# Optimization experiments

Measured on AMD Instinct MI355X. Metric: run time of the kernel, lower is better.

Reference implementation:

```python
import jax, jax.numpy as jnp
import numpy as np

HEADS = 8
K = 3            # kernel_size per axis
RPB = 2 * K - 1  # rel-pos-bias extent per axis
EPS = 1e-5


def _nbr(dim, k):
    # NATTEN-style clamped window: shift window to stay fully inside [0, dim)
    q = jnp.arange(dim)
    start = jnp.clip(q - k // 2, 0, dim - k)
    nbr = start[:, None] + jnp.arange(k)[None, :]       # (dim, k) neighbor coords
    rel = nbr - q[:, None] + (k - 1)                    # (dim, k) in [0, 2k-2]
    return nbr, rel


def _instance_norm(x):
    # InstanceNorm3d, affine=False: normalize over spatial dims per (B, C)
    m = jnp.mean(x, axis=(2, 3, 4), keepdims=True)
    v = jnp.var(x, axis=(2, 3, 4), keepdims=True)
    return (x - m) * jax.lax.rsqrt(v + EPS)


def setup_inputs() -> dict:
    key = jax.random.key(0)
    ks = jax.random.split(key, 10)
    B, C, H, W, Z = 1, 128, 32, 32, 32
    Cf = 4 * C
    s = 0.02
    return {
        "x": jax.random.normal(ks[0], (B, C, H, W, Z), jnp.float32),
        "w_qkv": jax.random.normal(ks[1], (3 * C, C), jnp.float32) * s,
        "b_qkv": jnp.zeros((3 * C,), jnp.float32),
        "rpb": jax.random.normal(ks[2], (HEADS, RPB, RPB, RPB), jnp.float32) * s,
        "w_proj": jax.random.normal(ks[3], (C, C), jnp.float32) * s,
        "b_proj": jnp.zeros((C,), jnp.float32),
        "w_ffn1": jax.random.normal(ks[4], (Cf, C), jnp.float32) * s,
        "b_ffn1": jnp.zeros((Cf,), jnp.float32),
        "w_ffn2": jax.random.normal(ks[5], (C, Cf), jnp.float32) * s,
        "b_ffn2": jnp.zeros((C,), jnp.float32),
    }


def reference(x, w_qkv, b_qkv, rpb, w_proj, b_proj, w_ffn1, b_ffn1, w_ffn2, b_ffn2):
    B, C, H, W, Z = x.shape
    hd = C // HEADS
    N = H * W * Z
    KK = K ** 3

    # ---- SAM: 3D neighborhood self-attention ----
    xt = x.reshape(B, C, N).transpose(0, 2, 1)                 # (B, N, C)
    qkv = xt @ w_qkv.T + b_qkv                                  # (B, N, 3C)
    q, k_, v = jnp.split(qkv, 3, axis=-1)
    split = lambda t: t.reshape(B, N, HEADS, hd).transpose(0, 2, 1, 3)  # (B, h, N, d)
    q, k_, v = split(q), split(k_), split(v)

    nh, rh = _nbr(H, K)
    nw, rw = _nbr(W, K)
    nz, rz = _nbr(Z, K)
    # flat neighbor token index per (h, w, z, kh, kw, kz)
    nbr = ((nh[:, None, None, :, None, None] * W
            + nw[None, :, None, None, :, None]) * Z
           + nz[None, None, :, None, None, :]).reshape(N, KK)   # (N, 27)
    # flat rel-pos-bias index
    bidx = ((rh[:, None, None, :, None, None] * RPB
             + rw[None, :, None, None, :, None]) * RPB
            + rz[None, None, :, None, None, :]).reshape(N, KK)  # (N, 27)

    kg = k_[:, :, nbr]                                          # (B, h, N, 27, d)
    vg = v[:, :, nbr]                                           # (B, h, N, 27, d)
    bias = rpb.reshape(HEADS, RPB ** 3)[:, bidx]                # (h, N, 27)

    scale = jnp.asarray(hd, x.dtype) ** -0.5
    attn = jnp.einsum('bhnd,bhnkd->bhnk', q * scale, kg) + bias
    attn = jax.nn.softmax(attn, axis=-1)
    out = jnp.einsum('bhnk,bhnkd->bhnd', attn, vg)              # (B, h, N, d)
    out = out.transpose(0, 2, 1, 3).reshape(B, N, C) @ w_proj.T + b_proj
    x5 = out.transpose(0, 2, 1).reshape(B, C, H, W, Z)

    # ---- norm_in ----
    x5 = _instance_norm(x5)

    # ---- FFN (mmcv-style, GELU, residual identity) ----
    t = x5.reshape(B, C, N).transpose(0, 2, 1)                  # (B, N, C)
    t = t + (jax.nn.gelu(t @ w_ffn1.T + b_ffn1) @ w_ffn2.T + b_ffn2)
    x5 = t.transpose(0, 2, 1).reshape(B, C, H, W, Z)

    # ---- norm_out ----
    return _instance_norm(x5)
```

## Files before the change

### kernel.cpp

```cpp
#include <hip/hip_runtime.h>
#include <hip/hip_bf16.h>
#include <math.h>

#define NPOS 32768
#define CCH  128
#define C3   384
#define CF   512
#define NSH  16

typedef __attribute__((ext_vector_type(8))) short short8;
typedef __attribute__((ext_vector_type(4))) float f32x4;

__device__ inline float bf2f(unsigned short u) {
    union { unsigned int i; float f; } x; x.i = ((unsigned int)u) << 16; return x.f;
}
__device__ inline unsigned short f2bf(float f) {
    union { float f; unsigned int i; } x; x.f = f;
    unsigned int r = x.i + 0x7FFFu + ((x.i >> 16) & 1u);
    return (unsigned short)(r >> 16);
}
__device__ inline float lo_bf(unsigned int u) {
    union { unsigned int i; float f; } x; x.i = u << 16; return x.f;
}
__device__ inline float hi_bf(unsigned int u) {
    union { unsigned int i; float f; } x; x.i = u & 0xffff0000u; return x.f;
}

template<bool GELU, bool RES, bool WF32, bool WBF>
__global__ __launch_bounds__(256) void gemm_mfma(
    const unsigned short* __restrict__ A, const unsigned short* __restrict__ B,
    const float* __restrict__ bias, const unsigned short* __restrict__ res,
    float* __restrict__ outf, unsigned short* __restrict__ outb,
    int M, int Nout, int K)
{
    __shared__ alignas(16) unsigned short As[128 * 40];
    __shared__ alignas(16) unsigned short Bs[128 * 40];

    const int tid  = threadIdx.x;
    const int lane = tid & 63;
    const int wave = tid >> 6;
    const int wm = wave & 1, wn = wave >> 1;
    const int row0 = blockIdx.y * 128;
    const int col0 = blockIdx.x * 128;

    const f32x4 fzero = {0.f, 0.f, 0.f, 0.f};
    f32x4 acc[4][4];
    #pragma unroll
    for (int i = 0; i < 4; ++i)
        #pragma unroll
        for (int j = 0; j < 4; ++j) acc[i][j] = fzero;

    const int lr = lane & 15;
    const int lk = (lane >> 4) * 8;

    for (int kt = 0; kt < K; kt += 32) {
        #pragma unroll
        for (int it = 0; it < 2; ++it) {
            const int c = tid + it * 256;
            const int r = c >> 2;
            const int p = (c & 3) * 8;
            *(uint4*)&As[r * 40 + p] = *(const uint4*)&A[(size_t)(row0 + r) * K + kt + p];
            *(uint4*)&Bs[r * 40 + p] = *(const uint4*)&B[(size_t)(col0 + r) * K + kt + p];
        }
        __syncthreads();
        short8 af[4], bfr[4];
        #pragma unroll
        for (int i = 0; i < 4; ++i)
            af[i]  = *(const short8*)&As[(wm * 64 + i * 16 + lr) * 40 + lk];
        #pragma unroll
        for (int j = 0; j < 4; ++j)
            bfr[j] = *(const short8*)&Bs[(wn * 64 + j * 16 + lr) * 40 + lk];
        #pragma unroll
        for (int i = 0; i < 4; ++i)
            #pragma unroll
            for (int j = 0; j < 4; ++j)
                acc[i][j] = __builtin_amdgcn_mfma_f32_16x16x32_bf16(
                                af[i], bfr[j], acc[i][j], 0, 0, 0);
        __syncthreads();
    }

    const int gr0 = row0 + wm * 64 + (lane >> 4) * 4;
    const int gc0 = col0 + wn * 64 + lr;
    #pragma unroll
    for (int j = 0; j < 4; ++j) {
        const int gc = gc0 + j * 16;
        const float bv = bias[gc];
        #pragma unroll
        for (int i = 0; i < 4; ++i) {
            #pragma unroll
            for (int r = 0; r < 4; ++r) {
                const int gr = gr0 + i * 16 + r;
                float v = acc[i][j][r] + bv;
                if (GELU) {
                    const float g = 0.7978845608028654f * (v + 0.044715f * v * v * v);
                    const float e = __expf(2.f * g);
                    v = v * (e / (e + 1.f));
                }
                if (RES)  v += bf2f(res[(size_t)gr * Nout + gc]);
                if (WF32) outf[(size_t)gr * Nout + gc] = v;
                if (WBF)  outb[(size_t)gr * Nout + gc] = f2bf(v);
            }
        }
    }
}

__global__ __launch_bounds__(256) void attn_tiled(
    const unsigned short* __restrict__ qkv, const float* __restrict__ rpb,
    unsigned short* __restrict__ out)
{
    __shared__ unsigned int ksu[288 * 8];
    __shared__ unsigned int vsu[288 * 8];
    __shared__ unsigned int qsu[32 * 8];
    __shared__ float logits[32 * 29];
    __shared__ float rpbs[125];
    __shared__ float sinv[32];

    const int t  = threadIdx.x;
    const int line = ((blockIdx.x & 7) << 7) + (blockIdx.x >> 3);
    const int h  = blockIdx.y;
    const int w0 = line & 31, h0 = line >> 5;
    const int n0 = (h0 << 10) + (w0 << 5);
    const int sh0 = min(max(h0 - 1, 0), 29);
    const int sw0 = min(max(w0 - 1, 0), 29);
    const int rh_off = sh0 - h0 + 2;
    const int rw_off = sw0 - w0 + 2;

    if (t < 64) {
        const int pos = t >> 1, part = t & 1;
        const uint4 raw = *(const uint4*)&qkv[(size_t)(n0 + pos) * C3 + h * 16 + part * 8];
        *(uint4*)&qsu[pos * 8 + part * 4] = raw;
    } else if (t < 192) {
        const int i = t - 64;
        if (i < 125) rpbs[i] = rpb[h * 125 + i];
    }
    for (int c = t; c < 1152; c += 256) {
        const int p = c >> 2, part = c & 3;
        const int ihw = p >> 5, z = p & 31;
        const int ih = (ihw * 11) >> 5;
        const int iw = ihw - 3 * ih;
        const int n = ((sh0 + ih) << 10) + ((sw0 + iw) << 5) + z;
        const uint4 raw = *(const uint4*)&qkv[(size_t)n * C3 + CCH + (part >> 1) * CCH
                                              + h * 16 + (part & 1) * 8];
        unsigned int* d = ((part < 2) ? ksu : vsu) + p * 8 + (part & 1) * 4;
        *(uint4*)d = raw;
    }
    __syncthreads();

    {
        const int q = t >> 3, j = t & 7;
        const int sz = min(max(q - 1, 0), 29);
        const int rz_off = sz - q + 2;
        float qf[16];
        #pragma unroll
        for (int d2 = 0; d2 < 8; ++d2) {
            const unsigned int u = qsu[q * 8 + d2];
            qf[2 * d2] = lo_bf(u); qf[2 * d2 + 1] = hi_bf(u);
        }
        float lv[4];
        int nkk = 0;
        for (int kk = j; kk < 27; kk += 8) {
            const int ihw = kk / 3, dz = kk - 3 * ihw;
            const int ih = ihw / 3,  iw = ihw - 3 * ih;
            const int p = ihw * 32 + sz + dz;
            float a = 0.f;
            #pragma unroll
            for (int d2 = 0; d2 < 8; ++d2) {
                const unsigned int u = ksu[p * 8 + d2];
                a += qf[2 * d2] * lo_bf(u) + qf[2 * d2 + 1] * hi_bf(u);
            }
            const int bidx = ((ih + rh_off) * 5 + (iw + rw_off)) * 5 + (dz + rz_off);
            lv[nkk++] = a * 0.25f + rpbs[bidx];
        }
        float mx = -1e30f;
        #pragma unroll
        for (int u = 0; u < 4; ++u) if (u < nkk) mx = fmaxf(mx, lv[u]);
        mx = fmaxf(mx, __shfl_xor(mx, 1));
        mx = fmaxf(mx, __shfl_xor(mx, 2));
        mx = fmaxf(mx, __shfl_xor(mx, 4));
        float s = 0.f;
        int u = 0;
        for (int kk = j; kk < 27; kk += 8) {
            const float e = __expf(lv[u++] - mx);
            logits[q * 29 + kk] = e;
            s += e;
        }
        s += __shfl_xor(s, 1);
        s += __shfl_xor(s, 2);
        s += __shfl_xor(s, 4);
        if (j == 0) sinv[q] = 1.f / s;
    }
    __syncthreads();

    {
        const int q = t >> 3, d2 = t & 7;
        const int sz = min(max(q - 1, 0), 29);
        float ax = 0.f, ay = 0.f;
        #pragma unroll
        for (int kk = 0; kk < 27; ++kk) {
            const int p = (kk / 3) * 32 + sz + (kk % 3);
            const float w = logits[q * 29 + kk];
            const unsigned int u = vsu[p * 8 + d2];
            ax += w * lo_bf(u); ay += w * hi_bf(u);
        }
        const float inv = sinv[q];
        const unsigned int o = ((unsigned int)f2bf(ay * inv) << 16)
                             |  (unsigned int)f2bf(ax * inv);
        *(unsigned int*)&out[(size_t)(n0 + q) * CCH + h * 16 + d2 * 2] = o;
    }
}

__global__ __launch_bounds__(256) void proj_stats_kernel(
    const unsigned short* __restrict__ attnO,
    const unsigned short* __restrict__ wproj,
    const float* __restrict__ b_proj,
    unsigned short* __restrict__ x5b,
    float* __restrict__ stats)
{
    __shared__ float red[256];

    const int t    = threadIdx.x;
    const int lane = t & 63;
    const int wn   = t >> 6;
    const int lr = lane & 15;
    const int lg = lane >> 4;
    const int lk = lg * 8;
    const int n0 = blockIdx.x * 64;
    const int sh = (blockIdx.x & (NSH - 1)) * 256;

    red[t] = 0.f;

    short8 wf[2][4];
    #pragma unroll
    for (int j = 0; j < 2; ++j)
        #pragma unroll
        for (int ks = 0; ks < 4; ++ks)
            wf[j][ks] = *(const short8*)&wproj[(wn * 32 + j * 16 + lr) * CCH + ks * 32 + lk];

    const f32x4 fzero = {0.f, 0.f, 0.f, 0.f};
    f32x4 acc[4][2];
    #pragma unroll
    for (int i = 0; i < 4; ++i)
        #pragma unroll
        for (int j = 0; j < 2; ++j) acc[i][j] = fzero;

    #pragma unroll
    for (int ks = 0; ks < 4; ++ks) {
        short8 af[4];
        #pragma unroll
        for (int i = 0; i < 4; ++i)
            af[i] = *(const short8*)&attnO[(size_t)(n0 + i * 16 + lr) * CCH + ks * 32 + lk];
        #pragma unroll
        for (int i = 0; i < 4; ++i)
            #pragma unroll
            for (int j = 0; j < 2; ++j)
                acc[i][j] = __builtin_amdgcn_mfma_f32_16x16x32_bf16(
                                af[i], wf[j][ks], acc[i][j], 0, 0, 0);
    }
    __syncthreads();

    #pragma unroll
    for (int j = 0; j < 2; ++j) {
        const int gc = wn * 32 + j * 16 + lr;
        const float bv = b_proj[gc];
        float s = 0.f, q = 0.f;
        #pragma unroll
        for (int i = 0; i < 4; ++i)
            #pragma unroll
            for (int r = 0; r < 4; ++r) {
                const int gr = i * 16 + lg * 4 + r;
                const float v = acc[i][j][r] + bv;
                s += v; q += v * v;
                x5b[(size_t)(n0 + gr) * CCH + gc] = f2bf(v);
            }
        atomicAdd(&red[gc], s);
        atomicAdd(&red[128 + gc], q);
    }
    __syncthreads();
    if (t < 128) {
        atomicAdd(&stats[sh + t],       red[t]);
        atomicAdd(&stats[sh + 128 + t], red[128 + t]);
    }
}

__global__ __launch_bounds__(256) void ffn_fused_kernel(
    const unsigned short* __restrict__ x5b,
    const unsigned short* __restrict__ w1,
    const float* __restrict__ b1,
    const unsigned short* __restrict__ w2,
    const float* __restrict__ b2,
    float* __restrict__ stats,
    float* __restrict__ tT)
{
    __shared__ alignas(16) unsigned short pool[2 * 8704];
    unsigned short* As = pool;
    unsigned short* Hs = pool + 8704;
    __shared__ float red[256];
    __shared__ float ms[128];
    __shared__ float rss[128];

    const int t    = threadIdx.x;
    const int lane = t & 63;
    const int wn   = t >> 6;
    const int lr = lane & 15;
    const int lg = lane >> 4;
    const int lk = lg * 8;
    const int n0 = blockIdx.x * 64;
    const int sh = (blockIdx.x & (NSH - 1)) * 256;
    const float invN = 1.f / (float)NPOS;
    const f32x4 fzero = {0.f, 0.f, 0.f, 0.f};

    red[t] = 0.f;
    if (t < 128) {
        float s0 = 0.f, s1 = 0.f;
        #pragma unroll
        for (int s = 0; s < NSH; ++s) {
            s0 += stats[s * 256 + t];
            s1 += stats[s * 256 + 128 + t];
        }
        const float m = s0 * invN;
        const float v = s1 * invN - m * m;
        ms[t]  = m;
        rss[t] = rsqrtf(v + 1e-5f);
    }
    uint4 px[4];
    #pragma unroll
    for (int it = 0; it < 4; ++it) {
        const int idx = t + it * 256;
        const int row = idx >> 4, c0 = (idx & 15) * 8;
        px[it] = *(const uint4*)&x5b[(size_t)(n0 + row) * CCH + c0];
    }
    __syncthreads();

    #pragma unroll
    for (int it = 0; it < 4; ++it) {
        const int idx = t + it * 256;
        const int row = idx >> 4, c0 = (idx & 15) * 8;
        unsigned int u[4] = {px[it].x, px[it].y, px[it].z, px[it].w};
        #pragma unroll
        for (int p = 0; p < 4; ++p) {
            const int c = c0 + 2 * p;
            const float a = (lo_bf(u[p]) - ms[c])     * rss[c];
            const float b = (hi_bf(u[p]) - ms[c + 1]) * rss[c + 1];
            u[p] = ((unsigned int)f2bf(b) << 16) | (unsigned int)f2bf(a);
        }
        uint4 w; w.x = u[0]; w.y = u[1]; w.z = u[2]; w.w = u[3];
        *(uint4*)&As[row * 136 + c0] = w;
    }
    __syncthreads();

    f32x4 acc[4][2];
    #pragma unroll
    for (int i = 0; i < 4; ++i)
        #pragma unroll
        for (int j = 0; j < 2; ++j) acc[i][j] = fzero;

    #pragma unroll 1
    for (int cc = 0; cc < 4; ++cc) {
        short8 w1f[2][4];
        #pragma unroll
        for (int j = 0; j < 2; ++j)
            #pragma unroll
            for (int ks = 0; ks < 4; ++ks)
                w1f[j][ks] = *(const short8*)&w1[
                    (size_t)(cc * 128 + wn * 32 + j * 16 + lr) * CCH + ks * 32 + lk];

        f32x4 hacc[4][2];
        #pragma unroll
        for (int i = 0; i < 4; ++i)
            #pragma unroll
            for (int j = 0; j < 2; ++j) hacc[i][j] = fzero;
        #pragma unroll
        for (int ks = 0; ks < 4; ++ks) {
            short8 af[4];
            #pragma unroll
            for (int i = 0; i < 4; ++i)
                af[i] = *(const short8*)&As[(i * 16 + lr) * 136 + ks * 32 + lk];
            #pragma unroll
            for (int i = 0; i < 4; ++i)
                #pragma unroll
                for (int j = 0; j < 2; ++j)
                    hacc[i][j] = __builtin_amdgcn_mfma_f32_16x16x32_bf16(
                                    af[i], w1f[j][ks], hacc[i][j], 0, 0, 0);
        }

        short8 w2f[2][4];
        #pragma unroll
        for (int j = 0; j < 2; ++j)
            #pragma unroll
            for (int ks = 0; ks < 4; ++ks)
                w2f[j][ks] = *(const short8*)&w2[
                    (size_t)(wn * 32 + j * 16 + lr) * CF + cc * 128 + ks * 32 + lk];

        #pragma unroll
        for (int j = 0; j < 2; ++j) {
            const int gc = wn * 32 + j * 16 + lr;
            const float bv = b1[cc * 128 + gc];
            #pragma unroll
            for (int i = 0; i < 4; ++i)
                #pragma unroll
                for (int r = 0; r < 4; ++r) {
                    float v = hacc[i][j][r] + bv;
                    const float g = 0.7978845608028654f * (v + 0.044715f * v * v * v);
                    const float e = __expf(2.f * g);
                    v = v * (e / (e + 1.f));
                    Hs[(i * 16 + lg * 4 + r) * 136 + gc] = f2bf(v);
                }
        }
        __syncthreads();

        #pragma unroll
        for (int ks = 0; ks < 4; ++ks) {
            short8 af[4];
            #pragma unroll
            for (int i = 0; i < 4; ++i)
                af[i] = *(const short8*)&Hs[(i * 16 + lr) * 136 + ks * 32 + lk];
            #pragma unroll
            for (int i = 0; i < 4; ++i)
                #pragma unroll
                for (int j = 0; j < 2; ++j)
                    acc[i][j] = __builtin_amdgcn_mfma_f32_16x16x32_bf16(
                                    af[i], w2f[j][ks], acc[i][j], 0, 0, 0);
        }
        __syncthreads();
    }

    #pragma unroll
    for (int j = 0; j < 2; ++j) {
        const int gc = wn * 32 + j * 16 + lr;
        const float bv = b2[gc];
        float s = 0.f, q = 0.f;
        #pragma unroll
        for (int i = 0; i < 4; ++i)
            #pragma unroll
            for (int r = 0; r < 4; ++r) {
                const int gr = i * 16 + lg * 4 + r;
                const float v = acc[i][j][r] + bv + bf2f(As[gr * 136 + gc]);
                acc[i][j][r] = v;
                s += v; q += v * v;
            }
        atomicAdd(&red[gc], s);
        atomicAdd(&red[128 + gc], q);
    }
    __syncthreads();
    if (t < 128) {
        atomicAdd(&stats[4096 + sh + t],       red[t]);
        atomicAdd(&stats[4096 + sh + 128 + t], red[128 + t]);
    }

    float* tr = (float*)pool;
    #pragma unroll
    for (int j = 0; j < 2; ++j) {
        const int gc = wn * 32 + j * 16 + lr;
        #pragma unroll
        for (int i = 0; i < 4; ++i)
            #pragma unroll
            for (int r = 0; r < 4; ++r) {
                const int gr = i * 16 + lg * 4 + r;
                tr[gc * 68 + gr] = acc[i][j][r];
            }
    }
    __syncthreads();
    #pragma unroll
    for (int it = 0; it < 8; ++it) {
        const int idx = t + it * 256;
        const int c = idx >> 4, ch = (idx & 15) * 4;
        float4 o4;
        o4.x = tr[c * 68 + ch + 0];
        o4.y = tr[c * 68 + ch + 1];
        o4.z = tr[c * 68 + ch + 2];
        o4.w = tr[c * 68 + ch + 3];
        *(float4*)&tT[(size_t)c * NPOS + n0 + ch] = o4;
    }
}

__global__ __launch_bounds__(256) void norm2_apply_kernel(
    const float* __restrict__ tT, const float* __restrict__ stats,
    float* __restrict__ out)
{
    const int i = blockIdx.x * 256 + threadIdx.x;
    const size_t o = (size_t)i * 4;
    const int c = (int)(o >> 15);
    const float invN = 1.f / (float)NPOS;
    float s0 = 0.f, s1 = 0.f;
    #pragma unroll
    for (int s = 0; s < NSH; ++s) {
        s0 += stats[4096 + s * 256 + c];
        s1 += stats[4096 + s * 256 + 128 + c];
    }
    const float m  = s0 * invN;
    const float vr = s1 * invN - m * m;
    const float rs = rsqrtf(vr + 1e-5f);
    float4 v = ((const float4*)tT)[i];
    v.x = (v.x - m) * rs;
    v.y = (v.y - m) * rs;
    v.z = (v.z - m) * rs;
    v.w = (v.w - m) * rs;
    ((float4*)out)[i] = v;
}

__global__ __launch_bounds__(256) void prep_kernel(
    const float* __restrict__ wq, const float* __restrict__ wp,
    const float* __restrict__ w1, const float* __restrict__ w2,
    unsigned short* __restrict__ wq_b, unsigned short* __restrict__ wp_b,
    unsigned short* __restrict__ w1_b, unsigned short* __restrict__ w2_b,
    float* __restrict__ stats)
{
    const int i = blockIdx.x * 256 + threadIdx.x;
    if (blockIdx.x < 16) {
        stats[blockIdx.x * 512 + threadIdx.x] = 0.f;
        stats[blockIdx.x * 512 + 256 + threadIdx.x] = 0.f;
    }
    const float* src; unsigned short* dst; int off;
    if (i < 12288)      { src = wq; dst = wq_b; off = i; }
    else if (i < 16384) { src = wp; dst = wp_b; off = i - 12288; }
    else if (i < 32768) { src = w1; dst = w1_b; off = i - 16384; }
    else                { src = w2; dst = w2_b; off = i - 32768; }
    const float4 v = ((const float4*)src)[off];
    ushort4 o;
    o.x = f2bf(v.x); o.y = f2bf(v.y); o.z = f2bf(v.z); o.w = f2bf(v.w);
    ((ushort4*)dst)[off] = o;
}

__global__ __launch_bounds__(256) void transpose_x_kernel(
    const float* __restrict__ x, unsigned short* __restrict__ xt)
{
    __shared__ float tile[32][33];
    const int n0 = blockIdx.x * 32;
    const int c0 = blockIdx.y * 32;
    const int tx = threadIdx.x & 31;
    const int ty = threadIdx.x >> 5;
    for (int i = ty; i < 32; i += 8)
        tile[i][tx] = x[(size_t)(c0 + i) * NPOS + n0 + tx];
    __syncthreads();
    for (int i = ty; i < 32; i += 8)
        xt[(size_t)(n0 + i) * CCH + c0 + tx] = f2bf(tile[tx][i]);
}

extern "C" void kernel_launch(void* const* d_in, const int* in_sizes, int n_in,
                              void* d_out, int out_size, void* d_ws, size_t ws_size,
                              hipStream_t stream)
{
    const float* x      = (const float*)d_in[0];
    const float* w_qkv  = (const float*)d_in[1];
    const float* b_qkv  = (const float*)d_in[2];
    const float* rpb    = (const float*)d_in[3];
    const float* w_proj = (const float*)d_in[4];
    const float* b_proj = (const float*)d_in[5];
    const float* w_ffn1 = (const float*)d_in[6];
    const float* b_ffn1 = (const float*)d_in[7];
    const float* w_ffn2 = (const float*)d_in[8];
    const float* b_ffn2 = (const float*)d_in[9];
    float* out = (float*)d_out;

    char* ws = (char*)d_ws;
    unsigned short* xt_bf    = (unsigned short*)(ws + 0);
    unsigned short* qkv_bf   = (unsigned short*)(ws + 8388608);
    unsigned short* attnO_bf = (unsigned short*)(ws + 33554432);
    unsigned short* x5_bf    = (unsigned short*)(ws + 41943040);
    float*          tT       = (float*)(ws + 50331648);
    unsigned short* wqkv_bf  = (unsigned short*)(ws + 83886080);
    unsigned short* wproj_bf = (unsigned short*)(ws + 83984384);
    unsigned short* wffn1_bf = (unsigned short*)(ws + 84017152);
    unsigned short* wffn2_bf = (unsigned short*)(ws + 84148224);
    float*          stats    = (float*)(ws + 84279296);

    prep_kernel<<<192, 256, 0, stream>>>(w_qkv, w_proj, w_ffn1, w_ffn2,
                                         wqkv_bf, wproj_bf, wffn1_bf, wffn2_bf, stats);
    transpose_x_kernel<<<dim3(NPOS / 32, CCH / 32), 256, 0, stream>>>(x, xt_bf);

    gemm_mfma<false, false, false, true><<<dim3(C3 / 128, NPOS / 128), 256, 0, stream>>>(
        xt_bf, wqkv_bf, b_qkv, nullptr, nullptr, qkv_bf, NPOS, C3, CCH);

    attn_tiled<<<dim3(1024, 8), 256, 0, stream>>>(qkv_bf, rpb, attnO_bf);

    proj_stats_kernel<<<NPOS / 64, 256, 0, stream>>>(
        attnO_bf, wproj_bf, b_proj, x5_bf, stats);

    ffn_fused_kernel<<<NPOS / 64, 256, 0, stream>>>(
        x5_bf, wffn1_bf, b_ffn1, wffn2_bf, b_ffn2, stats, tT);

    norm2_apply_kernel<<<(NPOS * CCH / 4) / 256, 256, 0, stream>>>(tT, stats, out);
}
```

Baseline: 181.5 us.

## Store QKV head-major and keep FFN output in bf16 before final norm

The QKV GEMM now writes its output in a per-head, per-q/k/v planar layout (sel, position, 16 channels), so each attention block reads contiguous 32-byte rows for its head instead of strided slices of a 384-wide row. Separately, the FFN kernel stores its pre-norm output as bf16 rather than fp32, and the final normalization kernel reads bf16 and processes 8 elements per thread. This cuts the intermediate tensor's write and read traffic in half. The cost is extra rounding before the last instance norm, and 2-byte scattered stores in the GEMM epilogue that may coalesce less well.

```diff
diff --git a/kernel.cpp b/kernel.cpp
--- a/kernel.cpp
+++ b/kernel.cpp
@@ -26,12 +26,11 @@
     union { unsigned int i; float f; } x; x.i = u & 0xffff0000u; return x.f;
 }
 
-template<bool GELU, bool RES, bool WF32, bool WBF>
-__global__ __launch_bounds__(256) void gemm_mfma(
-    const unsigned short* __restrict__ A, const unsigned short* __restrict__ B,
-    const float* __restrict__ bias, const unsigned short* __restrict__ res,
-    float* __restrict__ outf, unsigned short* __restrict__ outb,
-    int M, int Nout, int K)
+__global__ __launch_bounds__(256) void qkv_gemm_kernel(
+    const unsigned short* __restrict__ A,
+    const unsigned short* __restrict__ B,
+    const float* __restrict__ bias,
+    unsigned short* __restrict__ outh)
 {
     __shared__ alignas(16) unsigned short As[128 * 40];
     __shared__ alignas(16) unsigned short Bs[128 * 40];
@@ -53,14 +52,14 @@
     const int lr = lane & 15;
     const int lk = (lane >> 4) * 8;
 
-    for (int kt = 0; kt < K; kt += 32) {
+    for (int kt = 0; kt < CCH; kt += 32) {
         #pragma unroll
         for (int it = 0; it < 2; ++it) {
             const int c = tid + it * 256;
             const int r = c >> 2;
             const int p = (c & 3) * 8;
-            *(uint4*)&As[r * 40 + p] = *(const uint4*)&A[(size_t)(row0 + r) * K + kt + p];
-            *(uint4*)&Bs[r * 40 + p] = *(const uint4*)&B[(size_t)(col0 + r) * K + kt + p];
+            *(uint4*)&As[r * 40 + p] = *(const uint4*)&A[(size_t)(row0 + r) * CCH + kt + p];
+            *(uint4*)&Bs[r * 40 + p] = *(const uint4*)&B[(size_t)(col0 + r) * CCH + kt + p];
         }
         __syncthreads();
         short8 af[4], bfr[4];
@@ -83,29 +82,24 @@
     const int gc0 = col0 + wn * 64 + lr;
     #pragma unroll
     for (int j = 0; j < 4; ++j) {
-        const int gc = gc0 + j * 16;
+        const int gc  = gc0 + j * 16;
+        const int sel = gc >> 4;
+        const int ch  = gc & 15;
         const float bv = bias[gc];
         #pragma unroll
         for (int i = 0; i < 4; ++i) {
             #pragma unroll
             for (int r = 0; r < 4; ++r) {
                 const int gr = gr0 + i * 16 + r;
-                float v = acc[i][j][r] + bv;
-                if (GELU) {
-                    const float g = 0.7978845608028654f * (v + 0.044715f * v * v * v);
-                    const float e = __expf(2.f * g);
-                    v = v * (e / (e + 1.f));
-                }
-                if (RES)  v += bf2f(res[(size_t)gr * Nout + gc]);
-                if (WF32) outf[(size_t)gr * Nout + gc] = v;
-                if (WBF)  outb[(size_t)gr * Nout + gc] = f2bf(v);
+                outh[((size_t)sel * NPOS + gr) * 16 + ch] = f2bf(acc[i][j][r] + bv);
             }
         }
     }
 }
 
 __global__ __launch_bounds__(256) void attn_tiled(
-    const unsigned short* __restrict__ qkv, const float* __restrict__ rpb,
+    const unsigned short* __restrict__ qkv,
+    const float* __restrict__ rpb,
     unsigned short* __restrict__ out)
 {
     __shared__ unsigned int ksu[288 * 8];
@@ -127,7 +121,7 @@
 
     if (t < 64) {
         const int pos = t >> 1, part = t & 1;
-        const uint4 raw = *(const uint4*)&qkv[(size_t)(n0 + pos) * C3 + h * 16 + part * 8];
+        const uint4 raw = *(const uint4*)&qkv[((size_t)h * NPOS + n0 + pos) * 16 + part * 8];
         *(uint4*)&qsu[pos * 8 + part * 4] = raw;
     } else if (t < 192) {
         const int i = t - 64;
@@ -139,9 +133,10 @@
         const int ih = (ihw * 11) >> 5;
         const int iw = ihw - 3 * ih;
         const int n = ((sh0 + ih) << 10) + ((sw0 + iw) << 5) + z;
-        const uint4 raw = *(const uint4*)&qkv[(size_t)n * C3 + CCH + (part >> 1) * CCH
-                                              + h * 16 + (part & 1) * 8];
-        unsigned int* d = ((part < 2) ? ksu : vsu) + p * 8 + (part & 1) * 4;
+        const int kv = part >> 1;
+        const uint4 raw = *(const uint4*)&qkv[((size_t)(8 + kv * 8 + h) * NPOS + n) * 16
+                                              + (part & 1) * 8];
+        unsigned int* d = ((kv == 0) ? ksu : vsu) + p * 8 + (part & 1) * 4;
         *(uint4*)d = raw;
     }
     __syncthreads();
@@ -289,7 +284,7 @@
     const unsigned short* __restrict__ w2,
     const float* __restrict__ b2,
     float* __restrict__ stats,
-    float* __restrict__ tT)
+    unsigned short* __restrict__ tTb)
 {
     __shared__ alignas(16) unsigned short pool[2 * 8704];
     unsigned short* As = pool;
@@ -464,21 +459,21 @@
     for (int it = 0; it < 8; ++it) {
         const int idx = t + it * 256;
         const int c = idx >> 4, ch = (idx & 15) * 4;
-        float4 o4;
-        o4.x = tr[c * 68 + ch + 0];
-        o4.y = tr[c * 68 + ch + 1];
-        o4.z = tr[c * 68 + ch + 2];
-        o4.w = tr[c * 68 + ch + 3];
-        *(float4*)&tT[(size_t)c * NPOS + n0 + ch] = o4;
+        ushort4 o4;
+        o4.x = f2bf(tr[c * 68 + ch + 0]);
+        o4.y = f2bf(tr[c * 68 + ch + 1]);
+        o4.z = f2bf(tr[c * 68 + ch + 2]);
+        o4.w = f2bf(tr[c * 68 + ch + 3]);
+        *(ushort4*)&tTb[(size_t)c * NPOS + n0 + ch] = o4;
     }
 }
 
 __global__ __launch_bounds__(256) void norm2_apply_kernel(
-    const float* __restrict__ tT, const float* __restrict__ stats,
+    const unsigned short* __restrict__ tTb, const float* __restrict__ stats,
     float* __restrict__ out)
 {
     const int i = blockIdx.x * 256 + threadIdx.x;
-    const size_t o = (size_t)i * 4;
+    const size_t o = (size_t)i * 8;
     const int c = (int)(o >> 15);
     const float invN = 1.f / (float)NPOS;
     float s0 = 0.f, s1 = 0.f;
@@ -490,12 +485,15 @@
     const float m  = s0 * invN;
     const float vr = s1 * invN - m * m;
     const float rs = rsqrtf(vr + 1e-5f);
-    float4 v = ((const float4*)tT)[i];
-    v.x = (v.x - m) * rs;
-    v.y = (v.y - m) * rs;
-    v.z = (v.z - m) * rs;
-    v.w = (v.w - m) * rs;
-    ((float4*)out)[i] = v;
+    const uint4 raw = *(const uint4*)&tTb[o];
+    const unsigned int u[4] = {raw.x, raw.y, raw.z, raw.w};
+    float4 o0, o1;
+    o0.x = (lo_bf(u[0]) - m) * rs; o0.y = (hi_bf(u[0]) - m) * rs;
+    o0.z = (lo_bf(u[1]) - m) * rs; o0.w = (hi_bf(u[1]) - m) * rs;
+    o1.x = (lo_bf(u[2]) - m) * rs; o1.y = (hi_bf(u[2]) - m) * rs;
+    o1.z = (lo_bf(u[3]) - m) * rs; o1.w = (hi_bf(u[3]) - m) * rs;
+    *(float4*)&out[o]     = o0;
+    *(float4*)&out[o + 4] = o1;
 }
 
 __global__ __launch_bounds__(256) void prep_kernel(
@@ -557,7 +555,7 @@
     unsigned short* qkv_bf   = (unsigned short*)(ws + 8388608);
     unsigned short* attnO_bf = (unsigned short*)(ws + 33554432);
     unsigned short* x5_bf    = (unsigned short*)(ws + 41943040);
-    float*          tT       = (float*)(ws + 50331648);
+    unsigned short* tTb      = (unsigned short*)(ws + 50331648);
     unsigned short* wqkv_bf  = (unsigned short*)(ws + 83886080);
     unsigned short* wproj_bf = (unsigned short*)(ws + 83984384);
     unsigned short* wffn1_bf = (unsigned short*)(ws + 84017152);
@@ -568,8 +566,8 @@
                                          wqkv_bf, wproj_bf, wffn1_bf, wffn2_bf, stats);
     transpose_x_kernel<<<dim3(NPOS / 32, CCH / 32), 256, 0, stream>>>(x, xt_bf);
 
-    gemm_mfma<false, false, false, true><<<dim3(C3 / 128, NPOS / 128), 256, 0, stream>>>(
-        xt_bf, wqkv_bf, b_qkv, nullptr, nullptr, qkv_bf, NPOS, C3, CCH);
+    qkv_gemm_kernel<<<dim3(C3 / 128, NPOS / 128), 256, 0, stream>>>(
+        xt_bf, wqkv_bf, b_qkv, qkv_bf);
 
     attn_tiled<<<dim3(1024, 8), 256, 0, stream>>>(qkv_bf, rpb, attnO_bf);
 
@@ -577,7 +575,7 @@
         attnO_bf, wproj_bf, b_proj, x5_bf, stats);
 
     ffn_fused_kernel<<<NPOS / 64, 256, 0, stream>>>(
-        x5_bf, wffn1_bf, b_ffn1, wffn2_bf, b_ffn2, stats, tT);
-
-    norm2_apply_kernel<<<(NPOS * CCH / 4) / 256, 256, 0, stream>>>(tT, stats, out);
-}
+        x5_bf, wffn1_bf, b_ffn1, wffn2_bf, b_ffn2, stats, tTb);
+
+    norm2_apply_kernel<<<(NPOS * CCH / 8) / 256, 256, 0, stream>>>(tTb, stats, out);
+}
```

After: 182.1 us. About the same (+0.3%).
